# Kernel tuning notes

Hardware: AMD Instinct MI355X
Metric: run time of the kernel (lower is better)

## Reference

```python
import jax, jax.numpy as jnp
import numpy as np

THRESH = 0.7
MIN_KEPT = 100000
IGNORE_INDEX = -100


def setup_inputs() -> dict:
    key = jax.random.key(0)
    k1, k2 = jax.random.split(key)
    B, C, H, W = 8, 19, 512, 512
    logits = jax.random.normal(k1, (B, C, H, W), dtype=jnp.float32)
    targets = jax.random.randint(k2, (B, H, W), 0, C, dtype=jnp.int64)
    return {"logits": logits, "targets": targets}


def reference(logits, targets):
    B, C, H, W = logits.shape
    # softmax over class dim, then log(p + eps) as in the original
    probs = jax.nn.softmax(logits, axis=1)
    log_probs = jnp.log(probs + 1e-7)
    mask = (targets != IGNORE_INDEX)
    # per-pixel NLL: gather log-prob of the target class
    gathered = jnp.take_along_axis(log_probs, targets[:, None, :, :], axis=1)[:, 0]  # [B,H,W]
    losses = -gathered * mask.astype(logits.dtype)                                   # [B,H,W]
    losses_flat = losses.reshape(B, -1)                                              # [B,HW]
    n_pix = losses_flat.shape[1]
    # threshold index is static (Python ints), matching torch code exactly
    thresh_idx = max(MIN_KEPT, int(n_pix * THRESH))
    thresh_idx = min(thresh_idx, n_pix - 1)
    sorted_losses = jnp.sort(losses_flat, axis=1)
    thresh = sorted_losses[:, thresh_idx]                                            # [B]
    selected = losses_flat > thresh[:, None]                                         # [B,HW] bool
    # Faithful to the original (buggy-looking) loop:
    #   selected_mask[i, targets[i].flatten()] = 1
    # i.e. target *values* are used as indices into the flattened HW axis.
    tgt_flat = targets.reshape(B, -1)  # values in [0, C)
    selected = jax.vmap(lambda s, t: s.at[t].set(True))(selected, tgt_flat)
    return selected.reshape(B, H, W).astype(jnp.float32)
```

## Files before the change

### kernel.cpp

```cpp
#include <hip/hip_runtime.h>

#define NB 8
#define NC 19
#define HW (512*512)
#define NPIX (NB*HW)
#define RANK 183500u
#define NBIN 4096
#define CAP  4096

__device__ __forceinline__ unsigned fkey(float f) {
    unsigned b = __float_as_uint(f);
    return (b & 0x80000000u) ? ~b : (b | 0x80000000u);
}
__device__ __forceinline__ float finv(unsigned u) {
    unsigned b = (u & 0x80000000u) ? (u & 0x7fffffffu) : ~u;
    return __uint_as_float(b);
}
__device__ __forceinline__ int bin_of(float l) {
    int b = (int)((l + 1.0f) * 224.0f);
    return b < 0 ? 0 : (b > NBIN - 1 ? NBIN - 1 : b);
}
__device__ __forceinline__ unsigned umn(unsigned a, unsigned b) { return a < b ? a : b; }
__device__ __forceinline__ unsigned umx(unsigned a, unsigned b) { return a > b ? a : b; }

__global__ __launch_bounds__(256) void losses_kernel(
    const float* __restrict__ logits, const int* __restrict__ targets,
    float* __restrict__ losses)
{
    const int blk = blockIdx.x;
    const int bb  = (blk * 256) >> 18;
    const int pp  = (blk * 256) & (HW - 1);
    const int tid = threadIdx.x;
    const float* base = logits + (size_t)bb * NC * HW + pp + tid;

    float x[NC];
    #pragma unroll
    for (int c = 0; c < NC; ++c) x[c] = base[(size_t)c * HW];

    const int t = targets[blk * 256 + tid];

    float m = x[0];
    #pragma unroll
    for (int c = 1; c < NC; ++c) m = fmaxf(m, x[c]);

    float s = 0.f, et = 0.f;
    #pragma unroll
    for (int c = 0; c < NC; ++c) {
        float e = expf(x[c] - m);
        s += e;
        if (c == t) et = e;
    }
    float o = 0.f;
    if (t >= 0 && t < NC) o = -logf(et / s + 1e-7f);
    losses[blk * 256 + tid] = o;
}

__global__ __launch_bounds__(256) void hist_kernel(
    const float* __restrict__ losses, const int* __restrict__ targets,
    unsigned* __restrict__ ghist, unsigned* __restrict__ present)
{
    __shared__ unsigned lh[NBIN];
    __shared__ unsigned pres;
    const int b = blockIdx.y;
    for (int j = threadIdx.x; j < NBIN; j += 256) lh[j] = 0;
    if (threadIdx.x == 0) pres = 0u;
    __syncthreads();
    const float4* L = reinterpret_cast<const float4*>(losses + (size_t)b * HW)
                      + (size_t)blockIdx.x * 1024;
    const int4* T = reinterpret_cast<const int4*>(targets + (size_t)b * HW)
                    + (size_t)blockIdx.x * 1024;
    unsigned bits = 0u;
    for (int j = threadIdx.x; j < 1024; j += 256) {
        float4 v = L[j];
        atomicAdd(&lh[bin_of(v.x)], 1u);
        atomicAdd(&lh[bin_of(v.y)], 1u);
        atomicAdd(&lh[bin_of(v.z)], 1u);
        atomicAdd(&lh[bin_of(v.w)], 1u);
        int4 tv = T[j];
        if (tv.x >= 0 && tv.x < NC) bits |= 1u << tv.x;
        if (tv.y >= 0 && tv.y < NC) bits |= 1u << tv.y;
        if (tv.z >= 0 && tv.z < NC) bits |= 1u << tv.z;
        if (tv.w >= 0 && tv.w < NC) bits |= 1u << tv.w;
    }
    #pragma unroll
    for (int o = 1; o < 64; o <<= 1) bits |= __shfl_xor(bits, o);
    if ((threadIdx.x & 63) == 0 && bits) atomicOr(&pres, bits);
    __syncthreads();
    unsigned* gh = ghist + b * NBIN;
    for (int j = threadIdx.x; j < NBIN; j += 256) {
        unsigned v = lh[j];
        if (v) atomicAdd(&gh[j], v);
    }
    if (threadIdx.x == 0 && pres) atomicOr(&present[b], pres);
}

__global__ void pick_kernel(const unsigned* __restrict__ ghist,
                            unsigned* __restrict__ info)
{
    __shared__ unsigned lh[NBIN];
    __shared__ unsigned ps[256];
    const int b = blockIdx.x;
    const unsigned* gh = ghist + b * NBIN;
    for (int j = threadIdx.x; j < NBIN; j += 256) lh[j] = gh[j];
    __syncthreads();
    unsigned s = 0;
    for (int j = 0; j < 16; ++j) s += lh[threadIdx.x * 16 + j];
    ps[threadIdx.x] = s;
    __syncthreads();
    if (threadIdx.x == 0) {
        unsigned cum = 0;
        int chunk = 0;
        while (chunk < 255 && cum + ps[chunk] <= RANK) { cum += ps[chunk]; ++chunk; }
        int T = chunk * 16;
        while (T < NBIN - 1 && cum + lh[T] <= RANK) { cum += lh[T]; ++T; }
        info[b * 2]     = (unsigned)T;
        info[b * 2 + 1] = RANK - cum;
    }
}

__global__ __launch_bounds__(256) void compact_kernel(
    const float* __restrict__ losses, const unsigned* __restrict__ info,
    unsigned* __restrict__ count, float* __restrict__ cand)
{
    const int b = blockIdx.y;
    const int T = (int)info[b * 2];
    const int lane = threadIdx.x & 63;
    const float4* L = reinterpret_cast<const float4*>(losses + (size_t)b * HW)
                      + (size_t)blockIdx.x * 1024;
    for (int j = threadIdx.x; j < 1024; j += 256) {
        float4 v = L[j];
        float vals[4] = {v.x, v.y, v.z, v.w};
        #pragma unroll
        for (int q = 0; q < 4; ++q) {
            float val = vals[q];
            bool sel = (bin_of(val) == T);
            unsigned long long msk = __ballot(sel);
            if (msk) {
                int leader = __ffsll(msk) - 1;
                int pre = __popcll(msk & ((1ull << lane) - 1ull));
                unsigned base = 0;
                if (lane == leader) base = atomicAdd(&count[b], (unsigned)__popcll(msk));
                base = (unsigned)__shfl((int)base, leader);
                if (sel) {
                    unsigned idx = base + (unsigned)pre;
                    if (idx < CAP) cand[b * CAP + idx] = val;
                }
            }
        }
    }
}

__global__ __launch_bounds__(256) void final_kernel(
    const float* __restrict__ cand, const unsigned* __restrict__ count,
    const unsigned* __restrict__ info, float* __restrict__ thresh)
{
    __shared__ unsigned kf[CAP];
    __shared__ unsigned h[512];
    __shared__ unsigned sub[2048];
    __shared__ unsigned red[8];
    __shared__ unsigned kmin_sh, shift_sh, sb_sh, r2_sh, cnt_sh;
    const int tid = threadIdx.x, b = blockIdx.x;
    unsigned k = count[b]; if (k > CAP) k = CAP;
    const unsigned r = info[b * 2 + 1];

    for (unsigned j = tid; j < k; j += 256) kf[j] = fkey(cand[b * CAP + j]);
    for (int j = tid; j < 512; j += 256) h[j] = 0;
    __syncthreads();

    unsigned lmin = 0xFFFFFFFFu, lmax = 0u;
    for (unsigned j = tid; j < k; j += 256) { unsigned v = kf[j]; lmin = umn(lmin, v); lmax = umx(lmax, v); }
    #pragma unroll
    for (int o = 1; o < 64; o <<= 1) {
        lmin = umn(lmin, (unsigned)__shfl_xor((int)lmin, o));
        lmax = umx(lmax, (unsigned)__shfl_xor((int)lmax, o));
    }
    if ((tid & 63) == 0) { red[tid >> 6] = lmin; red[4 + (tid >> 6)] = lmax; }
    __syncthreads();
    if (tid == 0) {
        unsigned mn = red[0], mx = red[4];
        for (int w = 1; w < 4; ++w) { mn = umn(mn, red[w]); mx = umx(mx, red[4 + w]); }
        unsigned spread = mx - mn;
        int bits = 32 - __clz((int)(spread | 1u));
        shift_sh = (unsigned)(bits > 9 ? bits - 9 : 0);
        kmin_sh = mn;
        cnt_sh = 0;
    }
    __syncthreads();
    const unsigned kmin = kmin_sh, shift = shift_sh;
    for (unsigned j = tid; j < k; j += 256) atomicAdd(&h[(kf[j] - kmin) >> shift], 1u);
    __syncthreads();
    if (tid == 0) {
        unsigned cum = 0; int sb = 0;
        while (sb < 511 && cum + h[sb] <= r) { cum += h[sb]; ++sb; }
        sb_sh = (unsigned)sb; r2_sh = r - cum;
    }
    __syncthreads();
    const unsigned sb = sb_sh;
    for (unsigned j = tid; j < k; j += 256) {
        if (((kf[j] - kmin) >> shift) == sb) {
            unsigned idx = atomicAdd(&cnt_sh, 1u);
            if (idx < 2048) sub[idx] = kf[j];
        }
    }
    __syncthreads();
    const unsigned k2 = umn(cnt_sh, 2048u), r2 = r2_sh;
    for (unsigned e = tid; e < k2; e += 256) {
        unsigned v = sub[e], less = 0, eq = 0;
        for (unsigned j = 0; j < k2; ++j) { unsigned u = sub[j]; less += (u < v); eq += (u == v); }
        if (less <= r2 && r2 < less + eq) thresh[b] = finv(v);
    }
}

__global__ __launch_bounds__(256) void emit_kernel(
    float* __restrict__ out, const float* __restrict__ thresh,
    const unsigned* __restrict__ present)
{
    int i4 = blockIdx.x * 256 + threadIdx.x;
    int i = i4 * 4;
    int b = i >> 18;
    int p = i & (HW - 1);
    float th = thresh[b];
    unsigned pm = present[b];
    float4 v = reinterpret_cast<float4*>(out)[i4];
    float4 o;
    o.x = ((v.x > th) || ((p + 0) < NC && ((pm >> (p + 0)) & 1u))) ? 1.f : 0.f;
    o.y = ((v.y > th) || ((p + 1) < NC && ((pm >> (p + 1)) & 1u))) ? 1.f : 0.f;
    o.z = ((v.z > th) || ((p + 2) < NC && ((pm >> (p + 2)) & 1u))) ? 1.f : 0.f;
    o.w = ((v.w > th) || ((p + 3) < NC && ((pm >> (p + 3)) & 1u))) ? 1.f : 0.f;
    reinterpret_cast<float4*>(out)[i4] = o;
}

extern "C" void kernel_launch(void* const* d_in, const int* in_sizes, int n_in,
                              void* d_out, int out_size, void* d_ws, size_t ws_size,
                              hipStream_t stream)
{
    const float* logits  = (const float*)d_in[0];
    const int*   targets = (const int*)d_in[1];
    float* out = (float*)d_out;

    char* ws = (char*)d_ws;
    unsigned* ghist   = (unsigned*)(ws);
    unsigned* count   = (unsigned*)(ws + 131072);
    unsigned* present = (unsigned*)(ws + 131104);
    unsigned* info    = (unsigned*)(ws + 131136);
    float*    thresh  = (float*)   (ws + 131200);
    float*    cand    = (float*)   (ws + 131232);

    hipMemsetAsync(d_ws, 0, 131232, stream);

    losses_kernel<<<NPIX / 256, 256, 0, stream>>>(logits, targets, out);
    hist_kernel<<<dim3(64, NB), 256, 0, stream>>>(out, targets, ghist, present);
    pick_kernel<<<NB, 256, 0, stream>>>(ghist, info);
    compact_kernel<<<dim3(64, NB), 256, 0, stream>>>(out, info, count, cand);
    final_kernel<<<NB, 256, 0, stream>>>(cand, count, info, thresh);
    emit_kernel<<<NPIX / 4 / 256, 256, 0, stream>>>(out, thresh, present);
}
```

Measured before the change: 115.3 us.

## Vectorize loss kernel to 4 pixels per thread and fold pick into compact

The loss kernel now has each thread load four pixels per class with inline-asm dwordx4 loads, waits on all of them at once, and writes float4 outputs, using a quarter of the blocks. The separate pick kernel is removed. Each compact block finds the threshold bin itself with a wave-shuffle prefix scan over the global histogram, and block 0 writes the info for the final kernel. This is meant to cut memory-instruction count and one kernel launch, at the cost of more registers per thread and redundant scans across the 64 blocks per image.

```diff
diff --git a/kernel.cpp b/kernel.cpp
--- a/kernel.cpp
+++ b/kernel.cpp
@@ -8,6 +8,8 @@
 #define NBIN 4096
 #define CAP  4096
 
+typedef float f32x4 __attribute__((ext_vector_type(4)));
+
 __device__ __forceinline__ unsigned fkey(float f) {
     unsigned b = __float_as_uint(f);
     return (b & 0x80000000u) ? ~b : (b | 0x80000000u);
@@ -23,36 +25,48 @@
 __device__ __forceinline__ unsigned umn(unsigned a, unsigned b) { return a < b ? a : b; }
 __device__ __forceinline__ unsigned umx(unsigned a, unsigned b) { return a > b ? a : b; }
 
-__global__ __launch_bounds__(256) void losses_kernel(
+__global__ __launch_bounds__(256, 3) void losses_kernel(
     const float* __restrict__ logits, const int* __restrict__ targets,
     float* __restrict__ losses)
 {
-    const int blk = blockIdx.x;
-    const int bb  = (blk * 256) >> 18;
-    const int pp  = (blk * 256) & (HW - 1);
-    const int tid = threadIdx.x;
-    const float* base = logits + (size_t)bb * NC * HW + pp + tid;
-
-    float x[NC];
-    #pragma unroll
-    for (int c = 0; c < NC; ++c) x[c] = base[(size_t)c * HW];
-
-    const int t = targets[blk * 256 + tid];
-
-    float m = x[0];
-    #pragma unroll
-    for (int c = 1; c < NC; ++c) m = fmaxf(m, x[c]);
-
-    float s = 0.f, et = 0.f;
-    #pragma unroll
-    for (int c = 0; c < NC; ++c) {
-        float e = expf(x[c] - m);
-        s += e;
-        if (c == t) et = e;
-    }
-    float o = 0.f;
-    if (t >= 0 && t < NC) o = -logf(et / s + 1e-7f);
-    losses[blk * 256 + tid] = o;
+    const int blk  = blockIdx.x;
+    const int pix0 = blk * 1024;
+    const int bb   = pix0 >> 18;
+    const int pp   = pix0 & (HW - 1);
+    const int tid  = threadIdx.x;
+    const float* base = logits + (size_t)bb * NC * HW + pp;
+    const unsigned voff = (unsigned)(tid * 16);
+
+    f32x4 x[19];
+    #pragma unroll
+    for (int c = 0; c < NC; ++c)
+        asm volatile("global_load_dwordx4 %0, %1, %2"
+                     : "=v"(x[c]) : "v"(voff), "s"(base + (size_t)c * HW));
+
+    int4 t4 = *reinterpret_cast<const int4*>(targets + pix0 + tid * 4);
+
+    asm volatile("s_waitcnt vmcnt(0)" ::: "memory");
+    __builtin_amdgcn_sched_barrier(0);
+
+    const int tt[4] = {t4.x, t4.y, t4.z, t4.w};
+    float oo[4];
+    #pragma unroll
+    for (int j = 0; j < 4; ++j) {
+        const int t = tt[j];
+        float m = x[0][j];
+        #pragma unroll
+        for (int c = 1; c < NC; ++c) m = fmaxf(m, x[c][j]);
+        float s = 0.f, et = 0.f;
+        #pragma unroll
+        for (int c = 0; c < NC; ++c) {
+            float e = expf(x[c][j] - m);
+            s += e;
+            if (c == t) et = e;
+        }
+        oo[j] = (t >= 0 && t < NC) ? -logf(et / s + 1e-7f) : 0.f;
+    }
+    *reinterpret_cast<float4*>(losses + pix0 + tid * 4) =
+        make_float4(oo[0], oo[1], oo[2], oo[3]);
 }
 
 __global__ __launch_bounds__(256) void hist_kernel(
@@ -94,40 +108,50 @@
     if (threadIdx.x == 0 && pres) atomicOr(&present[b], pres);
 }
 
-__global__ void pick_kernel(const unsigned* __restrict__ ghist,
-                            unsigned* __restrict__ info)
-{
-    __shared__ unsigned lh[NBIN];
-    __shared__ unsigned ps[256];
-    const int b = blockIdx.x;
+__global__ __launch_bounds__(256) void compact_kernel(
+    const float* __restrict__ losses, const unsigned* __restrict__ ghist,
+    unsigned* __restrict__ count, float* __restrict__ cand,
+    unsigned* __restrict__ info)
+{
+    __shared__ unsigned wsum[4], woff[4];
+    __shared__ unsigned sh_T, sh_r;
+    const int b = blockIdx.y;
+    const int tid = threadIdx.x;
+    const int lane = tid & 63, wid = tid >> 6;
     const unsigned* gh = ghist + b * NBIN;
-    for (int j = threadIdx.x; j < NBIN; j += 256) lh[j] = gh[j];
-    __syncthreads();
+
     unsigned s = 0;
-    for (int j = 0; j < 16; ++j) s += lh[threadIdx.x * 16 + j];
-    ps[threadIdx.x] = s;
-    __syncthreads();
-    if (threadIdx.x == 0) {
-        unsigned cum = 0;
-        int chunk = 0;
-        while (chunk < 255 && cum + ps[chunk] <= RANK) { cum += ps[chunk]; ++chunk; }
-        int T = chunk * 16;
-        while (T < NBIN - 1 && cum + lh[T] <= RANK) { cum += lh[T]; ++T; }
-        info[b * 2]     = (unsigned)T;
-        info[b * 2 + 1] = RANK - cum;
-    }
-}
-
-__global__ __launch_bounds__(256) void compact_kernel(
-    const float* __restrict__ losses, const unsigned* __restrict__ info,
-    unsigned* __restrict__ count, float* __restrict__ cand)
-{
-    const int b = blockIdx.y;
-    const int T = (int)info[b * 2];
-    const int lane = threadIdx.x & 63;
+    #pragma unroll
+    for (int j = 0; j < 16; ++j) s += gh[tid * 16 + j];
+    unsigned incl = s;
+    #pragma unroll
+    for (int o = 1; o < 64; o <<= 1) {
+        unsigned v = (unsigned)__shfl_up((int)incl, o);
+        if (lane >= o) incl += v;
+    }
+    if (lane == 63) wsum[wid] = incl;
+    __syncthreads();
+    if (tid == 0) { unsigned c = 0; for (int w = 0; w < 4; ++w) { woff[w] = c; c += wsum[w]; } }
+    __syncthreads();
+    unsigned excl = woff[wid] + incl - s;
+    if (RANK >= excl && RANK < excl + s) {
+        unsigned rr = RANK - excl, cum = 0;
+        for (int j = 0; j < 16; ++j) {
+            unsigned c = gh[tid * 16 + j];
+            if (cum + c > rr) {
+                sh_T = (unsigned)(tid * 16 + j); sh_r = rr - cum;
+                if (blockIdx.x == 0) { info[b * 2] = sh_T; info[b * 2 + 1] = sh_r; }
+                break;
+            }
+            cum += c;
+        }
+    }
+    __syncthreads();
+    const int T = (int)sh_T;
+
     const float4* L = reinterpret_cast<const float4*>(losses + (size_t)b * HW)
                       + (size_t)blockIdx.x * 1024;
-    for (int j = threadIdx.x; j < 1024; j += 256) {
+    for (int j = tid; j < 1024; j += 256) {
         float4 v = L[j];
         float vals[4] = {v.x, v.y, v.z, v.w};
         #pragma unroll
@@ -248,10 +272,9 @@
 
     hipMemsetAsync(d_ws, 0, 131232, stream);
 
-    losses_kernel<<<NPIX / 256, 256, 0, stream>>>(logits, targets, out);
+    losses_kernel<<<NPIX / 1024, 256, 0, stream>>>(logits, targets, out);
     hist_kernel<<<dim3(64, NB), 256, 0, stream>>>(out, targets, ghist, present);
-    pick_kernel<<<NB, 256, 0, stream>>>(ghist, info);
-    compact_kernel<<<dim3(64, NB), 256, 0, stream>>>(out, info, count, cand);
+    compact_kernel<<<dim3(64, NB), 256, 0, stream>>>(out, ghist, count, cand, info);
     final_kernel<<<NB, 256, 0, stream>>>(cand, count, info, thresh);
     emit_kernel<<<NPIX / 4 / 256, 256, 0, stream>>>(out, thresh, present);
 }
```

New measurement: 112.1 us. -2.8%, faster.
